# Kernel optimization log

Measured on AMD Instinct MI355X. Metric: run time of the kernel, lower is better.

Reference implementation:

```python
import jax, jax.numpy as jnp
import numpy as np
import math

DIM = 4096
N_HEADS = 32
N_KV_HEADS = 8
HEAD_DIM = DIM // N_HEADS
N_REP = N_HEADS // N_KV_HEADS
ROPE_BASE = 10000.0


def apply_rotary_emb(x):
    # x: [b, s, h, d] -> rotate pairs (LLaMA-style complex rotation)
    b, s, h, d = x.shape
    inv_freq = 1.0 / (ROPE_BASE ** (jnp.arange(0, d, 2, dtype=jnp.float32) / d))  # [d/2]
    pos = jnp.arange(s, dtype=jnp.float32)
    ang = pos[:, None] * inv_freq[None, :]          # [s, d/2]
    cos = jnp.cos(ang)[None, :, None, :]            # [1, s, 1, d/2]
    sin = jnp.sin(ang)[None, :, None, :]
    xr = x.reshape(b, s, h, d // 2, 2)
    x0, x1 = xr[..., 0], xr[..., 1]
    out = jnp.stack([x0 * cos - x1 * sin, x0 * sin + x1 * cos], axis=-1)
    return out.reshape(b, s, h, d)


def setup_inputs() -> dict:
    key = jax.random.key(0)
    ks = jax.random.split(key, 5)
    sc = 1.0 / math.sqrt(DIM)
    return {
        "x": jax.random.normal(ks[0], (2, 2048, DIM), dtype=jnp.float32),
        "Wq": jax.random.normal(ks[1], (DIM, N_HEADS * HEAD_DIM), dtype=jnp.float32) * sc,
        "Wk": jax.random.normal(ks[2], (DIM, N_KV_HEADS * HEAD_DIM), dtype=jnp.float32) * sc,
        "Wv": jax.random.normal(ks[3], (DIM, N_KV_HEADS * HEAD_DIM), dtype=jnp.float32) * sc,
        "Wo": jax.random.normal(ks[4], (N_HEADS * HEAD_DIM, DIM), dtype=jnp.float32) * sc,
    }


def reference(x, Wq, Wk, Wv, Wo):
    b, s, _ = x.shape
    xq = (x @ Wq).reshape(b, s, N_HEADS, HEAD_DIM)
    xk = (x @ Wk).reshape(b, s, N_KV_HEADS, HEAD_DIM)
    xv = (x @ Wv).reshape(b, s, N_KV_HEADS, HEAD_DIM)
    xq = apply_rotary_emb(xq)
    xk = apply_rotary_emb(xk)
    # GQA: repeat kv heads
    xk = jnp.repeat(xk, N_REP, axis=2)  # [b, s, H, d]
    xv = jnp.repeat(xv, N_REP, axis=2)
    scores = jnp.einsum('bqhd,bkhd->bhqk', xq, xk) / math.sqrt(HEAD_DIM)
    causal = jnp.tril(jnp.ones((s, s), dtype=bool))
    scores = jnp.where(causal[None, None], scores, -jnp.inf)
    probs = jax.nn.softmax(scores.astype(jnp.float32), axis=-1).astype(xq.dtype)
    out = jnp.einsum('bhqk,bkhd->bqhd', probs, xv).reshape(b, s, N_HEADS * HEAD_DIM)
    return out @ Wo  # dropout is identity in eval
```

## Files before the change

kernel.cpp:

```cpp
#include <hip/hip_runtime.h>
#include <hip/hip_bf16.h>

typedef __attribute__((ext_vector_type(8))) short short8;
typedef __attribute__((ext_vector_type(4))) float f32x4;

typedef const void __attribute__((address_space(1)))* gptr_t;
typedef void __attribute__((address_space(3)))* sptr_t;

static __device__ __forceinline__ void gload_lds16(const void* g, void* l) {
  __builtin_amdgcn_global_load_lds((gptr_t)g, (sptr_t)l, 16, 0, 0);
}

static __device__ __forceinline__ unsigned short f2bf(float f) {
  unsigned int u = __float_as_uint(f);
  unsigned int r = (u + 0x7fffu + ((u >> 16) & 1u)) >> 16;
  return (unsigned short)r;
}
static __device__ __forceinline__ float bf2f(unsigned short b) {
  return __uint_as_float(((unsigned int)b) << 16);
}
static __device__ __forceinline__ unsigned int cvt_pk_bf16(float lo, float hi) {
  unsigned int r;
  asm("v_cvt_pk_bf16_f32 %0, %1, %2" : "=v"(r) : "v"(lo), "v"(hi));
  return r;
}

__global__ void cvt_f32_to_bf16(const float* __restrict__ in,
                                unsigned short* __restrict__ out, int n) {
  int idx = blockIdx.x * blockDim.x + threadIdx.x;
  int stride = gridDim.x * blockDim.x;
  for (int i = idx * 4; i < n; i += stride * 4) {
    const float4 v = *reinterpret_cast<const float4*>(in + i);
    unsigned long long packed =
        (unsigned long long)f2bf(v.x) | ((unsigned long long)f2bf(v.y) << 16) |
        ((unsigned long long)f2bf(v.z) << 32) | ((unsigned long long)f2bf(v.w) << 48);
    *reinterpret_cast<unsigned long long*>(out + i) = packed;
  }
}

__global__ void cvt_transpose_bf16(const float* __restrict__ in,
                                   unsigned short* __restrict__ out, int K, int N) {
  __shared__ unsigned short tile[32][33];
  int kt = blockIdx.y * 32, nt = blockIdx.x * 32;
  int tx = threadIdx.x & 31;
  int ty = threadIdx.x >> 5;
  #pragma unroll
  for (int i = 0; i < 32; i += 8)
    tile[ty + i][tx] = f2bf(in[(size_t)(kt + ty + i) * N + nt + tx]);
  __syncthreads();
  #pragma unroll
  for (int i = 0; i < 32; i += 8)
    out[(size_t)(nt + ty + i) * K + kt + tx] = tile[tx][ty + i];
}

__global__ void transpose_v(const unsigned short* __restrict__ Vp,
                            unsigned short* __restrict__ VT, int vstride) {
  __shared__ unsigned short tile[32][33];
  int st = blockIdx.x * 32;
  int dt = blockIdx.y * 32;
  int bh = blockIdx.z;
  int b = bh >> 3, h = bh & 7;
  int tx = threadIdx.x & 31, ty = threadIdx.x >> 5;
  #pragma unroll
  for (int i = 0; i < 32; i += 8)
    tile[ty + i][tx] = Vp[(size_t)(b * 2048 + st + ty + i) * vstride + h * 128 + dt + tx];
  __syncthreads();
  #pragma unroll
  for (int i = 0; i < 32; i += 8)
    VT[(size_t)((b * 8 + h) * 128 + dt + ty + i) * 2048 + st + tx] = tile[tx][ty + i];
}

__global__ void rope_kernel(unsigned short* __restrict__ buf, int rows, int nheads,
                            int rowstride, float oscale) {
  int total = rows * nheads * 64;
  int idx = blockIdx.x * blockDim.x + threadIdx.x;
  if (idx >= total) return;
  int j = idx & 63;
  int hh = (idx >> 6) % nheads;
  int r = idx / (64 * nheads);
  int pos = r & 2047;
  float inv = expf(-(float)j * 0.14391157f);
  float ang = (float)pos * inv;
  float s, c;
  sincosf(ang, &s, &c);
  unsigned int* p =
      reinterpret_cast<unsigned int*>(buf + (size_t)r * rowstride + hh * 128 + 2 * j);
  unsigned int pv = *p;
  float x0 = bf2f((unsigned short)(pv & 0xffffu));
  float x1 = bf2f((unsigned short)(pv >> 16));
  float o0 = (x0 * c - x1 * s) * oscale;
  float o1 = (x0 * s + x1 * c) * oscale;
  *p = (unsigned int)f2bf(o0) | ((unsigned int)f2bf(o1) << 16);
}

static __device__ __forceinline__ void store_out(unsigned short* C, size_t idx, float v) {
  C[idx] = f2bf(v);
}
static __device__ __forceinline__ void store_out(float* C, size_t idx, float v) {
  C[idx] = v;
}

template <int AM, typename OutT>
__global__ __launch_bounds__(512) void gemm_bt256(const unsigned short* __restrict__ A,
                                                  const unsigned short* __restrict__ BT,
                                                  OutT* __restrict__ C, int M, int N,
                                                  int K) {
  constexpr int H = AM / 4;
  __shared__ __align__(16) unsigned short S[4][(AM + 16) * 512];
  const int tid = threadIdx.x;
  const int w = tid >> 6, lane = tid & 63;
  const int fr = lane & 15, fg = lane >> 4;
  const int wr = w >> 2, wc = w & 3;

  const int nbx = N >> 8;
  const int bid = blockIdx.x;
  const int cpx = gridDim.x >> 3;
  const int lid = (bid & 7) * cpx + (bid >> 3);
  const int brow = lid / nbx, bcol = lid % nbx;

  const int srl = lane >> 2;
  const int scc = (lane & 3) ^ (((lane >> 5) & 1) << 1);
  const unsigned short* gA = A + (size_t)(brow * (AM * 16)) * K;
  const unsigned short* gB = BT + (size_t)(bcol * 256) * K;

  f32x4 acc[2 * H][4] = {};
  const int rdoff = fr * 32 + ((fg ^ (((fr >> 3) & 1) << 1)) * 8);

  const int NT = K >> 5;

  for (int s = 0; s < 3; s++) {
    const int kb = s * 32;
    #pragma unroll
    for (int u = 0; u < AM / 8; u++) {
      int sb = (AM / 8) * w + u;
      gload_lds16(gA + (size_t)(sb * 16 + srl) * K + kb + scc * 8, &S[s][sb * 512]);
    }
    #pragma unroll
    for (int u = 0; u < 2; u++) {
      int sb = 2 * w + u;
      gload_lds16(gB + (size_t)(sb * 16 + srl) * K + kb + scc * 8,
                  &S[s][AM * 512 + sb * 512]);
    }
  }
  if constexpr (AM == 16)
    asm volatile("s_waitcnt vmcnt(8)" ::: "memory");
  else
    asm volatile("s_waitcnt vmcnt(6)" ::: "memory");
  __builtin_amdgcn_s_barrier();

  for (int s = 0; s < NT; s++) {
    const unsigned short* Sa = &S[s & 3][0];
    const unsigned short* Sb = &S[s & 3][AM * 512];
    const int bufn = (s + 3) & 3;
    int kn = s + 3;
    if (kn >= NT) kn -= NT;
    const int kbn = kn * 32;

    short8 b[4], a0[H], a1[H];
    #pragma unroll
    for (int j = 0; j < 4; j++)
      b[j] = *reinterpret_cast<const short8*>(&Sb[(wc * 4 + j) * 512 + rdoff]);
    #pragma unroll
    for (int i = 0; i < H; i++)
      a0[i] = *reinterpret_cast<const short8*>(&Sa[(wr * 2 * H + i) * 512 + rdoff]);
    #pragma unroll
    for (int i = 0; i < H; i++)
      a1[i] = *reinterpret_cast<const short8*>(&Sa[(wr * 2 * H + H + i) * 512 + rdoff]);
    #pragma unroll
    for (int u = 0; u < AM / 8; u++) {
      int sb = (AM / 8) * w + u;
      gload_lds16(gA + (size_t)(sb * 16 + srl) * K + kbn + scc * 8, &S[bufn][sb * 512]);
    }
    #pragma unroll
    for (int u = 0; u < 2; u++) {
      int sb = 2 * w + u;
      gload_lds16(gB + (size_t)(sb * 16 + srl) * K + kbn + scc * 8,
                  &S[bufn][AM * 512 + sb * 512]);
    }
    if constexpr (AM == 16)
      asm volatile("s_waitcnt lgkmcnt(4)" ::: "memory");
    else
      asm volatile("s_waitcnt lgkmcnt(2)" ::: "memory");
    __builtin_amdgcn_sched_barrier(0);
    __builtin_amdgcn_s_setprio(1);
    #pragma unroll
    for (int i = 0; i < H; i++)
      #pragma unroll
      for (int j = 0; j < 4; j++)
        acc[i][j] = __builtin_amdgcn_mfma_f32_16x16x32_bf16(a0[i], b[j], acc[i][j], 0, 0, 0);
    __builtin_amdgcn_s_setprio(0);
    __builtin_amdgcn_sched_barrier(0);
    asm volatile("s_waitcnt lgkmcnt(0)" ::: "memory");
    __builtin_amdgcn_sched_barrier(0);
    __builtin_amdgcn_s_setprio(1);
    #pragma unroll
    for (int i = 0; i < H; i++)
      #pragma unroll
      for (int j = 0; j < 4; j++)
        acc[H + i][j] =
            __builtin_amdgcn_mfma_f32_16x16x32_bf16(a1[i], b[j], acc[H + i][j], 0, 0, 0);
    __builtin_amdgcn_s_setprio(0);
    if constexpr (AM == 16)
      asm volatile("s_waitcnt vmcnt(8)" ::: "memory");
    else
      asm volatile("s_waitcnt vmcnt(6)" ::: "memory");
    __builtin_amdgcn_s_barrier();
  }

  #pragma unroll
  for (int i = 0; i < 2 * H; i++)
    #pragma unroll
    for (int j = 0; j < 4; j++)
      #pragma unroll
      for (int r = 0; r < 4; r++) {
        int row = brow * (AM * 16) + wr * (AM * 8) + i * 16 + fg * 4 + r;
        int col = bcol * 256 + wc * 64 + j * 16 + fr;
        store_out(C, (size_t)row * N + col, acc[i][j][r]);
      }
}

__global__ __launch_bounds__(256, 2) void flash_attn(const unsigned short* __restrict__ Q,
                                                     const unsigned short* __restrict__ KV,
                                                     const unsigned short* __restrict__ VT,
                                                     unsigned short* __restrict__ O) {
  __shared__ __align__(16) unsigned short K_lds[2][64][128];
  __shared__ __align__(16) unsigned short V_lds[2][128][64];
  __shared__ __align__(16) unsigned short P_lds[4][16][68];

  const int wave = threadIdx.x >> 6, lane = threadIdx.x & 63;
  const int fr = lane & 15, fg = lane >> 4;

  const int bid = blockIdx.x;
  const int lid = (bid & 7) * 64 + (bid >> 3);
  const int pr = lid & 7;
  const int h = (lid >> 3) & 31;
  const int b = lid >> 8;
  const int kvh = h >> 2;

  const unsigned short* Qb = Q + (size_t)(b * 2048) * 4096 + h * 128;
  const unsigned short* Kb = KV + (size_t)(b * 2048) * 2048 + kvh * 128;
  const unsigned short* Vb = VT + (size_t)((b * 8 + kvh) * 128) * 2048;

  const int l4 = lane >> 4, c16 = lane & 15;
  const int l3 = lane >> 3, c8 = lane & 7;

  auto stage = [&](int kb, int bf) {
    #pragma unroll
    for (int c = 0; c < 4; c++) {
      int rl = wave * 16 + c * 4 + l4;
      int ch = c16 ^ (rl & 7);
      gload_lds16(Kb + (size_t)(kb + rl) * 2048 + ch * 8, &K_lds[bf][wave * 16 + c * 4][0]);
    }
    #pragma unroll
    for (int c = 0; c < 4; c++) {
      int rl = wave * 32 + c * 8 + l3;
      int ch = c8 ^ (rl & 7);
      gload_lds16(Vb + (size_t)rl * 2048 + kb + ch * 8, &V_lds[bf][wave * 32 + c * 8][0]);
    }
  };

  for (int seg = 0; seg < 2; seg++) {
    const int blk = seg ? pr : 15 - pr;
    const int qw = blk * 128 + wave * 32;

    short8 qf[2][4];
    #pragma unroll
    for (int m = 0; m < 2; m++)
      #pragma unroll
      for (int dk = 0; dk < 4; dk++)
        qf[m][dk] = *reinterpret_cast<const short8*>(
            &Qb[(size_t)(qw + m * 16 + fr) * 4096 + dk * 32 + fg * 8]);

    float mrow[2] = {-INFINITY, -INFINITY};
    float lrow[2] = {0.f, 0.f};
    f32x4 oacc[2][8] = {};

    const int nt = 2 * blk + 2;
    stage(0, 0);

    for (int t = 0; t < nt; t++) {
      const int kb = t * 64;
      if (t + 1 < nt) {
        stage((t + 1) * 64, (t + 1) & 1);
        asm volatile("s_waitcnt vmcnt(8)" ::: "memory");
      } else {
        asm volatile("s_waitcnt vmcnt(0)" ::: "memory");
      }
      __builtin_amdgcn_s_barrier();

      if (kb <= qw + 31) {
        const unsigned short* Kl = &K_lds[t & 1][0][0];
        const unsigned short* Vl = &V_lds[t & 1][0][0];

        f32x4 s[2][4] = {};
        #pragma unroll
        for (int kc = 0; kc < 4; kc++) {
          short8 kf[4];
          #pragma unroll
          for (int dk = 0; dk < 4; dk++)
            kf[dk] = *reinterpret_cast<const short8*>(
                &Kl[(kc * 16 + fr) * 128 + (((dk * 4 + fg) ^ (fr & 7)) << 3)]);
          #pragma unroll
          for (int dk = 0; dk < 4; dk++) {
            s[0][kc] =
                __builtin_amdgcn_mfma_f32_16x16x32_bf16(kf[dk], qf[0][dk], s[0][kc], 0, 0, 0);
            s[1][kc] =
                __builtin_amdgcn_mfma_f32_16x16x32_bf16(kf[dk], qf[1][dk], s[1][kc], 0, 0, 0);
          }
        }
        if (kb + 63 > qw) {
          #pragma unroll
          for (int m = 0; m < 2; m++) {
            const int qi = qw + m * 16 + fr;
            #pragma unroll
            for (int kc = 0; kc < 4; kc++)
              #pragma unroll
              for (int r = 0; r < 4; r++)
                if (kb + kc * 16 + fg * 4 + r > qi) s[m][kc][r] = -INFINITY;
          }
        }

        short8 pf[2][2];
        #pragma unroll
        for (int m = 0; m < 2; m++) {
          float mx = -INFINITY;
          #pragma unroll
          for (int kc = 0; kc < 4; kc++)
            #pragma unroll
            for (int r = 0; r < 4; r++) mx = fmaxf(mx, s[m][kc][r]);
          mx = fmaxf(mx, __shfl_xor(mx, 16));
          mx = fmaxf(mx, __shfl_xor(mx, 32));
          const bool need = !__all(mx - mrow[m] <= 8.0f);
          float mnew = need ? fmaxf(mrow[m], mx) : mrow[m];
          if (need) {
            float alpha = exp2f(mrow[m] - mnew);
            lrow[m] *= alpha;
            float alw[4];
            #pragma unroll
            for (int r = 0; r < 4; r++) alw[r] = __shfl(alpha, fg * 4 + r);
            #pragma unroll
            for (int dt = 0; dt < 8; dt++)
              #pragma unroll
              for (int r = 0; r < 4; r++) oacc[m][dt][r] *= alw[r];
          }
          float p_[16];
          float rs = 0.f;
          #pragma unroll
          for (int kc = 0; kc < 4; kc++)
            #pragma unroll
            for (int r = 0; r < 4; r++) {
              float pv = exp2f(s[m][kc][r] - mnew);
              p_[kc * 4 + r] = pv;
              rs += pv;
            }
          rs += __shfl_xor(rs, 16);
          rs += __shfl_xor(rs, 32);
          lrow[m] += rs;
          mrow[m] = mnew;
          #pragma unroll
          for (int kc = 0; kc < 4; kc++) {
            unsigned int lo = cvt_pk_bf16(p_[kc * 4 + 0], p_[kc * 4 + 1]);
            unsigned int hi = cvt_pk_bf16(p_[kc * 4 + 2], p_[kc * 4 + 3]);
            unsigned int* dst =
                reinterpret_cast<unsigned int*>(&P_lds[wave][fr][kc * 16 + fg * 4]);
            dst[0] = lo;
            dst[1] = hi;
          }
          pf[m][0] = *reinterpret_cast<const short8*>(&P_lds[wave][fr][fg * 8]);
          pf[m][1] = *reinterpret_cast<const short8*>(&P_lds[wave][fr][32 + fg * 8]);
        }

        #pragma unroll
        for (int c = 0; c < 2; c++)
          #pragma unroll
          for (int dt = 0; dt < 8; dt++) {
            short8 vf = *reinterpret_cast<const short8*>(
                &Vl[(dt * 16 + fr) * 64 + (((c * 4 + fg) ^ (fr & 7)) << 3)]);
            oacc[0][dt] =
                __builtin_amdgcn_mfma_f32_16x16x32_bf16(pf[0][c], vf, oacc[0][dt], 0, 0, 0);
            oacc[1][dt] =
                __builtin_amdgcn_mfma_f32_16x16x32_bf16(pf[1][c], vf, oacc[1][dt], 0, 0, 0);
          }
      }
      __builtin_amdgcn_s_barrier();
    }

    #pragma unroll
    for (int m = 0; m < 2; m++) {
      float linv[4];
      #pragma unroll
      for (int r = 0; r < 4; r++) linv[r] = 1.0f / __shfl(lrow[m], fg * 4 + r);
      #pragma unroll
      for (int dt = 0; dt < 8; dt++)
        #pragma unroll
        for (int r = 0; r < 4; r++) {
          int row = qw + m * 16 + fg * 4 + r;
          float v = oacc[m][dt][r] * linv[r];
          O[(size_t)(b * 2048 + row) * 4096 + h * 128 + dt * 16 + fr] = f2bf(v);
        }
    }
  }
}

extern "C" void kernel_launch(void* const* d_in, const int* in_sizes, int n_in,
                              void* d_out, int out_size, void* d_ws, size_t ws_size,
                              hipStream_t stream) {
  const float* x = (const float*)d_in[0];
  const float* Wq = (const float*)d_in[1];
  const float* Wk = (const float*)d_in[2];
  const float* Wv = (const float*)d_in[3];
  const float* Wo = (const float*)d_in[4];
  float* out = (float*)d_out;

  char* ws = (char*)d_ws;
  unsigned short* xb   = (unsigned short*)(ws + 0);
  unsigned short* WqT  = (unsigned short*)(ws + 33554432);
  unsigned short* WkvT = (unsigned short*)(ws + 67108864);
  unsigned short* WoT  = (unsigned short*)(ws + 83886080);
  unsigned short* Qb   = (unsigned short*)(ws + 117440512);
  unsigned short* KVb  = (unsigned short*)(ws + 150994944);
  unsigned short* VT   = (unsigned short*)(ws + 167772160);
  unsigned short* Ob   = (unsigned short*)(ws + 176160768);

  cvt_f32_to_bf16<<<2048, 256, 0, stream>>>(x, xb, 4096 * 4096);
  cvt_transpose_bf16<<<dim3(128, 128), 256, 0, stream>>>(Wq, WqT, 4096, 4096);
  cvt_transpose_bf16<<<dim3(32, 128), 256, 0, stream>>>(Wk, WkvT, 4096, 1024);
  cvt_transpose_bf16<<<dim3(32, 128), 256, 0, stream>>>(Wv, WkvT + (size_t)1024 * 4096,
                                                        4096, 1024);
  cvt_transpose_bf16<<<dim3(128, 128), 256, 0, stream>>>(Wo, WoT, 4096, 4096);

  gemm_bt256<16, unsigned short><<<256, 512, 0, stream>>>(xb, WqT, Qb, 4096, 4096, 4096);
  gemm_bt256<8, unsigned short><<<256, 512, 0, stream>>>(xb, WkvT, KVb, 4096, 2048, 4096);

  rope_kernel<<<(4096 * 32 * 64 + 255) / 256, 256, 0, stream>>>(Qb, 4096, 32, 4096,
                                                                0.12751780f);
  rope_kernel<<<(4096 * 8 * 64 + 255) / 256, 256, 0, stream>>>(KVb, 4096, 8, 2048, 1.0f);

  transpose_v<<<dim3(64, 4, 16), 256, 0, stream>>>(KVb + 1024, VT, 2048);

  flash_attn<<<512, 256, 0, stream>>>(Qb, KVb, VT, Ob);

  gemm_bt256<16, float><<<256, 512, 0, stream>>>(Ob, WoT, out, 4096, 4096, 4096);
}
```

Baseline: 516.3 us.

## Fuse Q RoPE into flash attention and read V directly from global

```diff
diff --git a/kernel.cpp b/kernel.cpp
--- a/kernel.cpp
+++ b/kernel.cpp
@@ -219,12 +219,11 @@
       }
 }
 
-__global__ __launch_bounds__(256, 2) void flash_attn(const unsigned short* __restrict__ Q,
+__global__ __launch_bounds__(256, 4) void flash_attn(const unsigned short* __restrict__ Q,
                                                      const unsigned short* __restrict__ KV,
                                                      const unsigned short* __restrict__ VT,
                                                      unsigned short* __restrict__ O) {
   __shared__ __align__(16) unsigned short K_lds[2][64][128];
-  __shared__ __align__(16) unsigned short V_lds[2][128][64];
   __shared__ __align__(16) unsigned short P_lds[4][16][68];
 
   const int wave = threadIdx.x >> 6, lane = threadIdx.x & 63;
@@ -242,7 +241,6 @@
   const unsigned short* Vb = VT + (size_t)((b * 8 + kvh) * 128) * 2048;
 
   const int l4 = lane >> 4, c16 = lane & 15;
-  const int l3 = lane >> 3, c8 = lane & 7;
 
   auto stage = [&](int kb, int bf) {
     #pragma unroll
@@ -251,12 +249,28 @@
       int ch = c16 ^ (rl & 7);
       gload_lds16(Kb + (size_t)(kb + rl) * 2048 + ch * 8, &K_lds[bf][wave * 16 + c * 4][0]);
     }
-    #pragma unroll
-    for (int c = 0; c < 4; c++) {
-      int rl = wave * 32 + c * 8 + l3;
-      int ch = c8 ^ (rl & 7);
-      gload_lds16(Vb + (size_t)rl * 2048 + kb + ch * 8, &V_lds[bf][wave * 32 + c * 8][0]);
-    }
+  };
+
+  auto load_rope_q = [&](int row, int dk) -> short8 {
+    const uint4 raw = *reinterpret_cast<const uint4*>(
+        &Qb[(size_t)row * 4096 + dk * 32 + fg * 8]);
+    unsigned int ws[4] = {raw.x, raw.y, raw.z, raw.w};
+    short8 out;
+    unsigned int* op = reinterpret_cast<unsigned int*>(&out);
+    #pragma unroll
+    for (int e = 0; e < 4; e++) {
+      const int j = dk * 16 + fg * 4 + e;
+      float inv = expf(-(float)j * 0.14391157f);
+      float ang = (float)row * inv;
+      float sn, cs;
+      sincosf(ang, &sn, &cs);
+      float x0 = bf2f((unsigned short)(ws[e] & 0xffffu));
+      float x1 = bf2f((unsigned short)(ws[e] >> 16));
+      float o0 = (x0 * cs - x1 * sn) * 0.12751780f;
+      float o1 = (x0 * sn + x1 * cs) * 0.12751780f;
+      op[e] = cvt_pk_bf16(o0, o1);
+    }
+    return out;
   };
 
   for (int seg = 0; seg < 2; seg++) {
@@ -268,8 +282,7 @@
     for (int m = 0; m < 2; m++)
       #pragma unroll
       for (int dk = 0; dk < 4; dk++)
-        qf[m][dk] = *reinterpret_cast<const short8*>(
-            &Qb[(size_t)(qw + m * 16 + fr) * 4096 + dk * 32 + fg * 8]);
+        qf[m][dk] = load_rope_q(qw + m * 16 + fr, dk);
 
     float mrow[2] = {-INFINITY, -INFINITY};
     float lrow[2] = {0.f, 0.f};
@@ -282,7 +295,7 @@
       const int kb = t * 64;
       if (t + 1 < nt) {
         stage((t + 1) * 64, (t + 1) & 1);
-        asm volatile("s_waitcnt vmcnt(8)" ::: "memory");
+        asm volatile("s_waitcnt vmcnt(4)" ::: "memory");
       } else {
         asm volatile("s_waitcnt vmcnt(0)" ::: "memory");
       }
@@ -290,7 +303,6 @@
 
       if (kb <= qw + 31) {
         const unsigned short* Kl = &K_lds[t & 1][0][0];
-        const unsigned short* Vl = &V_lds[t & 1][0][0];
 
         f32x4 s[2][4] = {};
         #pragma unroll
@@ -375,7 +387,7 @@
           #pragma unroll
           for (int dt = 0; dt < 8; dt++) {
             short8 vf = *reinterpret_cast<const short8*>(
-                &Vl[(dt * 16 + fr) * 64 + (((c * 4 + fg) ^ (fr & 7)) << 3)]);
+                &Vb[(size_t)(dt * 16 + fr) * 2048 + kb + c * 32 + fg * 8]);
             oacc[0][dt] =
                 __builtin_amdgcn_mfma_f32_16x16x32_bf16(pf[0][c], vf, oacc[0][dt], 0, 0, 0);
             oacc[1][dt] =
@@ -432,8 +444,6 @@
   gemm_bt256<16, unsigned short><<<256, 512, 0, stream>>>(xb, WqT, Qb, 4096, 4096, 4096);
   gemm_bt256<8, unsigned short><<<256, 512, 0, stream>>>(xb, WkvT, KVb, 4096, 2048, 4096);
 
-  rope_kernel<<<(4096 * 32 * 64 + 255) / 256, 256, 0, stream>>>(Qb, 4096, 32, 4096,
-                                                                0.12751780f);
   rope_kernel<<<(4096 * 8 * 64 + 255) / 256, 256, 0, stream>>>(KVb, 4096, 8, 2048, 1.0f);
 
   transpose_v<<<dim3(64, 4, 16), 256, 0, stream>>>(KVb + 1024, VT, 2048);
```

Result: slower. 691.7 us (+34.0%).

## Single-buffer V tile and shrink P scratch to fit three attention blocks per CU

Applied to the files above, without the earlier changes.

```diff
diff --git a/kernel.cpp b/kernel.cpp
--- a/kernel.cpp
+++ b/kernel.cpp
@@ -219,13 +219,13 @@
       }
 }
 
-__global__ __launch_bounds__(256, 2) void flash_attn(const unsigned short* __restrict__ Q,
+__global__ __launch_bounds__(256, 3) void flash_attn(const unsigned short* __restrict__ Q,
                                                      const unsigned short* __restrict__ KV,
                                                      const unsigned short* __restrict__ VT,
                                                      unsigned short* __restrict__ O) {
   __shared__ __align__(16) unsigned short K_lds[2][64][128];
-  __shared__ __align__(16) unsigned short V_lds[2][128][64];
-  __shared__ __align__(16) unsigned short P_lds[4][16][68];
+  __shared__ __align__(16) unsigned short V_lds[128][64];
+  __shared__ __align__(16) unsigned short P_lds[4][16][36];
 
   const int wave = threadIdx.x >> 6, lane = threadIdx.x & 63;
   const int fr = lane & 15, fg = lane >> 4;
@@ -244,18 +244,20 @@
   const int l4 = lane >> 4, c16 = lane & 15;
   const int l3 = lane >> 3, c8 = lane & 7;
 
-  auto stage = [&](int kb, int bf) {
+  auto stageK = [&](int kb, int bf) {
     #pragma unroll
     for (int c = 0; c < 4; c++) {
       int rl = wave * 16 + c * 4 + l4;
       int ch = c16 ^ (rl & 7);
       gload_lds16(Kb + (size_t)(kb + rl) * 2048 + ch * 8, &K_lds[bf][wave * 16 + c * 4][0]);
     }
+  };
+  auto stageV = [&](int kb) {
     #pragma unroll
     for (int c = 0; c < 4; c++) {
       int rl = wave * 32 + c * 8 + l3;
       int ch = c8 ^ (rl & 7);
-      gload_lds16(Vb + (size_t)rl * 2048 + kb + ch * 8, &V_lds[bf][wave * 32 + c * 8][0]);
+      gload_lds16(Vb + (size_t)rl * 2048 + kb + ch * 8, &V_lds[wave * 32 + c * 8][0]);
     }
   };
 
@@ -276,22 +278,24 @@
     f32x4 oacc[2][8] = {};
 
     const int nt = 2 * blk + 2;
-    stage(0, 0);
+    stageK(0, 0);
 
     for (int t = 0; t < nt; t++) {
       const int kb = t * 64;
+      __builtin_amdgcn_s_barrier();
+      stageV(kb);
       if (t + 1 < nt) {
-        stage((t + 1) * 64, (t + 1) & 1);
+        stageK((t + 1) * 64, (t + 1) & 1);
         asm volatile("s_waitcnt vmcnt(8)" ::: "memory");
       } else {
-        asm volatile("s_waitcnt vmcnt(0)" ::: "memory");
+        asm volatile("s_waitcnt vmcnt(4)" ::: "memory");
       }
       __builtin_amdgcn_s_barrier();
 
-      if (kb <= qw + 31) {
+      const bool work = (kb <= qw + 31);
+      short8 pf[2][2];
+      if (work) {
         const unsigned short* Kl = &K_lds[t & 1][0][0];
-        const unsigned short* Vl = &V_lds[t & 1][0][0];
-
         f32x4 s[2][4] = {};
         #pragma unroll
         for (int kc = 0; kc < 4; kc++) {
@@ -320,7 +324,6 @@
           }
         }
 
-        short8 pf[2][2];
         #pragma unroll
         for (int m = 0; m < 2; m++) {
           float mx = -INFINITY;
@@ -358,31 +361,41 @@
           lrow[m] += rs;
           mrow[m] = mnew;
           #pragma unroll
-          for (int kc = 0; kc < 4; kc++) {
-            unsigned int lo = cvt_pk_bf16(p_[kc * 4 + 0], p_[kc * 4 + 1]);
-            unsigned int hi = cvt_pk_bf16(p_[kc * 4 + 2], p_[kc * 4 + 3]);
-            unsigned int* dst =
-                reinterpret_cast<unsigned int*>(&P_lds[wave][fr][kc * 16 + fg * 4]);
-            dst[0] = lo;
-            dst[1] = hi;
+          for (int half = 0; half < 2; half++) {
+            #pragma unroll
+            for (int kc = 0; kc < 2; kc++) {
+              int kk = half * 2 + kc;
+              unsigned int lo = cvt_pk_bf16(p_[kk * 4 + 0], p_[kk * 4 + 1]);
+              unsigned int hi = cvt_pk_bf16(p_[kk * 4 + 2], p_[kk * 4 + 3]);
+              unsigned int* dst =
+                  reinterpret_cast<unsigned int*>(&P_lds[wave][fr][kc * 16 + fg * 4]);
+              dst[0] = lo;
+              dst[1] = hi;
+            }
+            pf[m][half] = *reinterpret_cast<const short8*>(&P_lds[wave][fr][fg * 8]);
           }
-          pf[m][0] = *reinterpret_cast<const short8*>(&P_lds[wave][fr][fg * 8]);
-          pf[m][1] = *reinterpret_cast<const short8*>(&P_lds[wave][fr][32 + fg * 8]);
         }
-
+      }
+
+      if (t + 1 < nt)
+        asm volatile("s_waitcnt vmcnt(4)" ::: "memory");
+      else
+        asm volatile("s_waitcnt vmcnt(0)" ::: "memory");
+      __builtin_amdgcn_s_barrier();
+
+      if (work) {
         #pragma unroll
         for (int c = 0; c < 2; c++)
           #pragma unroll
           for (int dt = 0; dt < 8; dt++) {
             short8 vf = *reinterpret_cast<const short8*>(
-                &Vl[(dt * 16 + fr) * 64 + (((c * 4 + fg) ^ (fr & 7)) << 3)]);
+                &V_lds[dt * 16 + fr][(((c * 4 + fg) ^ (fr & 7)) << 3)]);
             oacc[0][dt] =
                 __builtin_amdgcn_mfma_f32_16x16x32_bf16(pf[0][c], vf, oacc[0][dt], 0, 0, 0);
             oacc[1][dt] =
                 __builtin_amdgcn_mfma_f32_16x16x32_bf16(pf[1][c], vf, oacc[1][dt], 0, 0, 0);
           }
       }
-      __builtin_amdgcn_s_barrier();
     }
 
     #pragma unroll
```

After: 581.5 us. 1.13x slower.

## Add 8-phase pipelined 256x256 GEMM for Q and output projections

Applied to the files above, without the earlier changes.

```diff
diff --git a/kernel.cpp b/kernel.cpp
--- a/kernel.cpp
+++ b/kernel.cpp
@@ -100,6 +100,118 @@
   C[idx] = v;
 }
 
+template <typename OutT>
+__global__ __launch_bounds__(512) void gemm_8ph(const unsigned short* __restrict__ A,
+                                                const unsigned short* __restrict__ BT,
+                                                OutT* __restrict__ C, int M, int N,
+                                                int K) {
+  __shared__ __align__(16) unsigned short S[2][4][8192];
+  const int tid = threadIdx.x;
+  const int w = tid >> 6, lane = tid & 63;
+  const int fr = lane & 15, fg = lane >> 4;
+  const int wr = w >> 2, wc = w & 3;
+
+  const int nbx = N >> 8;
+  const int bid = blockIdx.x;
+  const int cpx = gridDim.x >> 3;
+  const int lid = (bid & 7) * cpx + (bid >> 3);
+  const int brow = lid / nbx, bcol = lid % nbx;
+
+  const int sr8 = lane >> 3;
+  const int sc8 = lane & 7;
+  const int sgc = sc8 ^ sr8;
+  const unsigned short* gA = A + (size_t)(brow * 256) * K;
+  const unsigned short* gB = BT + (size_t)(bcol * 256) * K;
+  const int NT = K >> 6;
+
+  f32x4 acc[8][4] = {};
+
+  auto stageHT = [&](int t, int ht) {
+    if (t >= NT) t -= NT;
+    const unsigned short* src = (ht < 2) ? gA : gB;
+    const int half = ht & 1;
+    unsigned short* dst = &S[t & 1][ht][0];
+    #pragma unroll
+    for (int l = 0; l < 2; l++) {
+      const int rl = w * 16 + l * 8;
+      gload_lds16(src + (size_t)(half * 128 + rl + sr8) * K + t * 64 + sgc * 8,
+                  dst + rl * 64);
+    }
+  };
+
+  stageHT(0, 0);
+  stageHT(0, 1);
+  stageHT(0, 2);
+  stageHT(0, 3);
+  stageHT(1, 2);
+  stageHT(1, 3);
+  asm volatile("s_waitcnt vmcnt(4)" ::: "memory");
+  __builtin_amdgcn_s_barrier();
+
+  const int rdswz = fr & 7;
+  for (int t = 0; t < NT; t++) {
+    const unsigned short* Sa = &S[t & 1][wr][0];
+    const unsigned short* Sb = &S[t & 1][2 + (wc >> 1)][0];
+    short8 bfr[4][2];
+    #pragma unroll
+    for (int q = 0; q < 4; q++) {
+      short8 a[2][2];
+      #pragma unroll
+      for (int i = 0; i < 2; i++)
+        #pragma unroll
+        for (int ks = 0; ks < 2; ks++) {
+          const int row = (2 * q + i) * 16 + fr;
+          a[i][ks] = *reinterpret_cast<const short8*>(
+              &Sa[row * 64 + ((ks * 4 + fg) ^ rdswz) * 8]);
+        }
+      if (q == 0) {
+        #pragma unroll
+        for (int n = 0; n < 4; n++)
+          #pragma unroll
+          for (int ks = 0; ks < 2; ks++) {
+            const int row = (wc & 1) * 64 + n * 16 + fr;
+            bfr[n][ks] = *reinterpret_cast<const short8*>(
+                &Sb[row * 64 + ((ks * 4 + fg) ^ rdswz) * 8]);
+          }
+      }
+      if (q < 2)
+        stageHT(t + 1, q);
+      else
+        stageHT(t + 2, q);
+      __builtin_amdgcn_s_barrier();
+      asm volatile("s_waitcnt lgkmcnt(0)" ::: "memory");
+      __builtin_amdgcn_sched_barrier(0);
+      __builtin_amdgcn_s_setprio(1);
+      #pragma unroll
+      for (int i = 0; i < 2; i++)
+        #pragma unroll
+        for (int n = 0; n < 4; n++) {
+          acc[2 * q + i][n] =
+              __builtin_amdgcn_mfma_f32_16x16x32_bf16(a[i][0], bfr[n][0],
+                                                      acc[2 * q + i][n], 0, 0, 0);
+          acc[2 * q + i][n] =
+              __builtin_amdgcn_mfma_f32_16x16x32_bf16(a[i][1], bfr[n][1],
+                                                      acc[2 * q + i][n], 0, 0, 0);
+        }
+      __builtin_amdgcn_s_setprio(0);
+      if (q == 3) asm volatile("s_waitcnt vmcnt(4)" ::: "memory");
+      __builtin_amdgcn_s_barrier();
+    }
+  }
+  asm volatile("s_waitcnt vmcnt(0)" ::: "memory");
+
+  #pragma unroll
+  for (int i = 0; i < 8; i++)
+    #pragma unroll
+    for (int n = 0; n < 4; n++)
+      #pragma unroll
+      for (int r = 0; r < 4; r++) {
+        int row = brow * 256 + wr * 128 + i * 16 + fg * 4 + r;
+        int col = bcol * 256 + wc * 64 + n * 16 + fr;
+        store_out(C, (size_t)row * N + col, acc[i][n][r]);
+      }
+}
+
 template <int AM, typename OutT>
 __global__ __launch_bounds__(512) void gemm_bt256(const unsigned short* __restrict__ A,
                                                   const unsigned short* __restrict__ BT,
@@ -142,10 +254,7 @@
                   &S[s][AM * 512 + sb * 512]);
     }
   }
-  if constexpr (AM == 16)
-    asm volatile("s_waitcnt vmcnt(8)" ::: "memory");
-  else
-    asm volatile("s_waitcnt vmcnt(6)" ::: "memory");
+  asm volatile("s_waitcnt vmcnt(6)" ::: "memory");
   __builtin_amdgcn_s_barrier();
 
   for (int s = 0; s < NT; s++) {
@@ -177,10 +286,7 @@
       gload_lds16(gB + (size_t)(sb * 16 + srl) * K + kbn + scc * 8,
                   &S[bufn][AM * 512 + sb * 512]);
     }
-    if constexpr (AM == 16)
-      asm volatile("s_waitcnt lgkmcnt(4)" ::: "memory");
-    else
-      asm volatile("s_waitcnt lgkmcnt(2)" ::: "memory");
+    asm volatile("s_waitcnt lgkmcnt(2)" ::: "memory");
     __builtin_amdgcn_sched_barrier(0);
     __builtin_amdgcn_s_setprio(1);
     #pragma unroll
@@ -200,10 +306,7 @@
         acc[H + i][j] =
             __builtin_amdgcn_mfma_f32_16x16x32_bf16(a1[i], b[j], acc[H + i][j], 0, 0, 0);
     __builtin_amdgcn_s_setprio(0);
-    if constexpr (AM == 16)
-      asm volatile("s_waitcnt vmcnt(8)" ::: "memory");
-    else
-      asm volatile("s_waitcnt vmcnt(6)" ::: "memory");
+    asm volatile("s_waitcnt vmcnt(6)" ::: "memory");
     __builtin_amdgcn_s_barrier();
   }
 
@@ -429,7 +532,7 @@
                                                         4096, 1024);
   cvt_transpose_bf16<<<dim3(128, 128), 256, 0, stream>>>(Wo, WoT, 4096, 4096);
 
-  gemm_bt256<16, unsigned short><<<256, 512, 0, stream>>>(xb, WqT, Qb, 4096, 4096, 4096);
+  gemm_8ph<unsigned short><<<256, 512, 0, stream>>>(xb, WqT, Qb, 4096, 4096, 4096);
   gemm_bt256<8, unsigned short><<<256, 512, 0, stream>>>(xb, WkvT, KVb, 4096, 2048, 4096);
 
   rope_kernel<<<(4096 * 32 * 64 + 255) / 256, 256, 0, stream>>>(Qb, 4096, 32, 4096,
@@ -440,5 +543,5 @@
 
   flash_attn<<<512, 256, 0, stream>>>(Qb, KVb, VT, Ob);
 
-  gemm_bt256<16, float><<<256, 512, 0, stream>>>(Ob, WoT, out, 4096, 4096, 4096);
-}
+  gemm_8ph<float><<<256, 512, 0, stream>>>(Ob, WoT, out, 4096, 4096, 4096);
+}
```

Result: no change. 510.9 us (-1.1%).
